# Optimization experiments

Hardware: AMD Instinct MI355X
Metric: run time of the kernel (lower is better)

Reference implementation:

```python
import jax, jax.numpy as jnp
import numpy as np

N, M_CODES, Z_DIM = 4096, 4096, 1024


def setup_inputs() -> dict:
    key = jax.random.key(0)
    k1, k2 = jax.random.split(key)
    z = jax.random.normal(k1, (N, Z_DIM), dtype=jnp.float32)
    e = jax.random.normal(k2, (M_CODES, Z_DIM), dtype=jnp.float32)
    return {"z": z, "e": e}


def reference(z, e):
    # Squared pairwise L2 distances [N, M] via GEMM expansion:
    # ||z_i - e_j||^2 = ||z_i||^2 + ||e_j||^2 - 2 z_i . e_j
    z_sq = jnp.sum(z * z, axis=1)               # [N]
    e_sq = jnp.sum(e * e, axis=1)               # [M]
    cross = jnp.einsum('nd,md->nm', z, e)       # [N, M]
    dist = z_sq[:, None] + e_sq[None, :] - 2.0 * cross  # [N, M]
    # min over dim 0 (over data points N) -> per-code nearest distance [M]
    loss = jnp.mean(jnp.min(dist, axis=0))
    return loss
```

## Files before the change

### kernel.cpp

```cpp
#include <hip/hip_runtime.h>
#include <hip/hip_bf16.h>
#include <stdint.h>

#define N_PTS   4096
#define M_CODES 4096
#define ZDIM    1024
#define BM 128
#define BN 128
#define BK 32

typedef __attribute__((ext_vector_type(8))) short bf16x8;
typedef __attribute__((ext_vector_type(4))) float f32x4;

__device__ __forceinline__ unsigned short f2bf(float f) {
    __hip_bfloat16 h = __float2bfloat16(f);
    return *reinterpret_cast<unsigned short*>(&h);
}

__device__ __forceinline__ unsigned enc_f32(float f) {
    unsigned u = __float_as_uint(f);
    return (u & 0x80000000u) ? ~u : (u | 0x80000000u);
}
__device__ __forceinline__ float dec_f32(unsigned e) {
    unsigned u = (e & 0x80000000u) ? (e ^ 0x80000000u) : ~e;
    return __uint_as_float(u);
}

__global__ __launch_bounds__(256) void prep_kernel(
    const float* __restrict__ z, const float* __restrict__ e,
    unsigned short* __restrict__ zb, unsigned short* __restrict__ eb,
    float* __restrict__ zsq, float* __restrict__ esq,
    unsigned* __restrict__ min_enc) {
    const int row = blockIdx.x;
    const int t = threadIdx.x;
    if (row < 16) min_enc[row * 256 + t] = 0xFFFFFFFFu;

    const float* src;
    unsigned short* dst;
    float* sqp;
    if (row < N_PTS) {
        src = z + (size_t)row * ZDIM; dst = zb + (size_t)row * ZDIM; sqp = zsq + row;
    } else {
        const int r = row - N_PTS;
        src = e + (size_t)r * ZDIM; dst = eb + (size_t)r * ZDIM; sqp = esq + r;
    }
    float4 v = reinterpret_cast<const float4*>(src)[t];
    ushort4 o;
    o.x = f2bf(v.x); o.y = f2bf(v.y); o.z = f2bf(v.z); o.w = f2bf(v.w);
    reinterpret_cast<ushort4*>(dst)[t] = o;
    float s = v.x * v.x + v.y * v.y + v.z * v.z + v.w * v.w;
    #pragma unroll
    for (int off = 32; off > 0; off >>= 1) s += __shfl_down(s, off, 64);
    __shared__ float red[4];
    if ((t & 63) == 0) red[t >> 6] = s;
    __syncthreads();
    if (t == 0) *sqp = red[0] + red[1] + red[2] + red[3];
}

__global__ __launch_bounds__(256) void gemm_min_kernel(
    const unsigned short* __restrict__ zb, const unsigned short* __restrict__ eb,
    const float* __restrict__ zsq, unsigned* __restrict__ min_enc) {
    __shared__ __align__(16) unsigned short As[BM * BK];
    __shared__ __align__(16) unsigned short Bs[BN * BK];
    __shared__ float zsq_s[BM];

    const int t = threadIdx.x;
    const int bx = blockIdx.x;
    const int by = blockIdx.y;
    const int lane = t & 63;
    const int w = t >> 6;
    const int wm = w >> 1, wn = w & 1;
    const int lrow = lane & 15;
    const int q = lane >> 4;

    if (t < BM) zsq_s[t] = zsq[by * BM + t];

    f32x4 acc[4][4];
    #pragma unroll
    for (int i = 0; i < 4; i++)
        #pragma unroll
        for (int j = 0; j < 4; j++) acc[i][j] = (f32x4){0.f, 0.f, 0.f, 0.f};

    const int row0 = (t * 16) >> 6;
    const int kel0 = ((t * 16) & 63) >> 1;
    const int lds_b0 = (t >> 6) * 512;
    const size_t a_base = (size_t)(by * BM) * ZDIM;
    const size_t b_base = (size_t)(bx * BN) * ZDIM;

    for (int k0 = 0; k0 < ZDIM; k0 += BK) {
        const unsigned short* ga0 = zb + a_base + (size_t)row0 * ZDIM + k0 + kel0;
        const unsigned short* gb0 = eb + b_base + (size_t)row0 * ZDIM + k0 + kel0;
        __builtin_amdgcn_global_load_lds(
            (const __attribute__((address_space(1))) void*)ga0,
            (__attribute__((address_space(3))) void*)(As + lds_b0), 16, 0, 0);
        __builtin_amdgcn_global_load_lds(
            (const __attribute__((address_space(1))) void*)(ga0 + (size_t)64 * ZDIM),
            (__attribute__((address_space(3))) void*)(As + 2048 + lds_b0), 16, 0, 0);
        __builtin_amdgcn_global_load_lds(
            (const __attribute__((address_space(1))) void*)gb0,
            (__attribute__((address_space(3))) void*)(Bs + lds_b0), 16, 0, 0);
        __builtin_amdgcn_global_load_lds(
            (const __attribute__((address_space(1))) void*)(gb0 + (size_t)64 * ZDIM),
            (__attribute__((address_space(3))) void*)(Bs + 2048 + lds_b0), 16, 0, 0);
        __syncthreads();

        bf16x8 a[4], b[4];
        #pragma unroll
        for (int am = 0; am < 4; am++)
            a[am] = *(const bf16x8*)(As + (wm * 64 + am * 16 + lrow) * BK + q * 8);
        #pragma unroll
        for (int an = 0; an < 4; an++)
            b[an] = *(const bf16x8*)(Bs + (wn * 64 + an * 16 + lrow) * BK + q * 8);
        #pragma unroll
        for (int am = 0; am < 4; am++)
            #pragma unroll
            for (int an = 0; an < 4; an++)
                acc[am][an] = __builtin_amdgcn_mfma_f32_16x16x32_bf16(
                    a[am], b[an], acc[am][an], 0, 0, 0);
        __syncthreads();
    }

    #pragma unroll
    for (int an = 0; an < 4; an++) {
        float v = 3.4e38f;
        #pragma unroll
        for (int am = 0; am < 4; am++) {
            const int rbase = wm * 64 + am * 16 + q * 4;
            f32x4 c = acc[am][an];
            v = fminf(v, zsq_s[rbase + 0] - 2.f * c[0]);
            v = fminf(v, zsq_s[rbase + 1] - 2.f * c[1]);
            v = fminf(v, zsq_s[rbase + 2] - 2.f * c[2]);
            v = fminf(v, zsq_s[rbase + 3] - 2.f * c[3]);
        }
        v = fminf(v, __shfl_xor(v, 16, 64));
        v = fminf(v, __shfl_xor(v, 32, 64));
        if (q == 0) {
            const int col = bx * BN + wn * 64 + an * 16 + lrow;
            atomicMin(&min_enc[col], enc_f32(v));
        }
    }
}

__global__ __launch_bounds__(256) void finalize_kernel(
    const unsigned* __restrict__ min_enc, const float* __restrict__ esq,
    float* __restrict__ out) {
    const int t = threadIdx.x;
    float s = 0.f;
    #pragma unroll
    for (int i = 0; i < M_CODES / 256; i++) {
        const int j = i * 256 + t;
        s += dec_f32(min_enc[j]) + esq[j];
    }
    #pragma unroll
    for (int off = 32; off > 0; off >>= 1) s += __shfl_down(s, off, 64);
    __shared__ float red[4];
    if ((t & 63) == 0) red[t >> 6] = s;
    __syncthreads();
    if (t == 0) out[0] = (red[0] + red[1] + red[2] + red[3]) * (1.f / M_CODES);
}

extern "C" void kernel_launch(void* const* d_in, const int* in_sizes, int n_in,
                              void* d_out, int out_size, void* d_ws, size_t ws_size,
                              hipStream_t stream) {
    (void)in_sizes; (void)n_in; (void)out_size; (void)ws_size;
    const float* z = (const float*)d_in[0];
    const float* e = (const float*)d_in[1];
    char* ws = (char*)d_ws;
    unsigned short* zb = (unsigned short*)ws;
    unsigned short* eb = (unsigned short*)(ws + ((size_t)8 << 20));
    float* zsq = (float*)(ws + ((size_t)16 << 20));
    float* esq = (float*)(ws + ((size_t)16 << 20) + 4096 * 4);
    unsigned* min_enc = (unsigned*)(ws + ((size_t)16 << 20) + 2 * 4096 * 4);

    prep_kernel<<<dim3(8192), dim3(256), 0, stream>>>(z, e, zb, eb, zsq, esq, min_enc);
    gemm_min_kernel<<<dim3(M_CODES / BN, N_PTS / BM), dim3(256), 0, stream>>>(
        zb, eb, zsq, min_enc);
    finalize_kernel<<<dim3(1), dim3(256), 0, stream>>>(min_enc, esq, (float*)d_out);
}
```

Baseline: 125.0 us.

## Double BK with swizzled LDS, fuse finalize via last-block counter, one-row-per-wave prep

Increases the K tile to 64 so each barrier pair covers twice the MFMA work, and adds an XOR swizzle on LDS chunk placement to avoid bank conflicts on the fragment reads. The per-block column minima are merged in shared memory before a single atomicMin per column. The separate finalize launch is removed, and the last block to finish (tracked by an atomic counter) computes the mean. The prep kernel now processes one row per wave, using a quarter of the blocks and no LDS reduction. This adds threadfence and counter overhead and doubles LDS use per block.

After: 186.0 us. +48.8%, slower.

```diff
diff --git a/kernel.cpp b/kernel.cpp
--- a/kernel.cpp
+++ b/kernel.cpp
@@ -7,7 +7,8 @@
 #define ZDIM    1024
 #define BM 128
 #define BN 128
-#define BK 32
+#define BK 64
+#define NBLOCKS ((N_PTS / BM) * (M_CODES / BN))
 
 typedef __attribute__((ext_vector_type(8))) short bf16x8;
 typedef __attribute__((ext_vector_type(4))) float f32x4;
@@ -30,11 +31,14 @@
     const float* __restrict__ z, const float* __restrict__ e,
     unsigned short* __restrict__ zb, unsigned short* __restrict__ eb,
     float* __restrict__ zsq, float* __restrict__ esq,
-    unsigned* __restrict__ min_enc) {
-    const int row = blockIdx.x;
+    unsigned* __restrict__ min_enc, unsigned* __restrict__ done_counter) {
     const int t = threadIdx.x;
-    if (row < 16) min_enc[row * 256 + t] = 0xFFFFFFFFu;
-
+    const int b = blockIdx.x;
+    if (b < 16) min_enc[b * 256 + t] = 0xFFFFFFFFu;
+    if (b == 16 && t == 0) *done_counter = 0u;
+
+    const int w = t >> 6, lane = t & 63;
+    const int row = b * 4 + w;
     const float* src;
     unsigned short* dst;
     float* sqp;
@@ -44,25 +48,33 @@
         const int r = row - N_PTS;
         src = e + (size_t)r * ZDIM; dst = eb + (size_t)r * ZDIM; sqp = esq + r;
     }
-    float4 v = reinterpret_cast<const float4*>(src)[t];
-    ushort4 o;
-    o.x = f2bf(v.x); o.y = f2bf(v.y); o.z = f2bf(v.z); o.w = f2bf(v.w);
-    reinterpret_cast<ushort4*>(dst)[t] = o;
-    float s = v.x * v.x + v.y * v.y + v.z * v.z + v.w * v.w;
-    #pragma unroll
-    for (int off = 32; off > 0; off >>= 1) s += __shfl_down(s, off, 64);
-    __shared__ float red[4];
-    if ((t & 63) == 0) red[t >> 6] = s;
-    __syncthreads();
-    if (t == 0) *sqp = red[0] + red[1] + red[2] + red[3];
+    const float4* s4 = reinterpret_cast<const float4*>(src);
+    ushort4* d4 = reinterpret_cast<ushort4*>(dst);
+    float s = 0.f;
+    #pragma unroll
+    for (int i = 0; i < 4; i++) {
+        float4 v = s4[i * 64 + lane];
+        ushort4 o;
+        o.x = f2bf(v.x); o.y = f2bf(v.y); o.z = f2bf(v.z); o.w = f2bf(v.w);
+        d4[i * 64 + lane] = o;
+        s += v.x * v.x + v.y * v.y + v.z * v.z + v.w * v.w;
+    }
+    #pragma unroll
+    for (int off = 1; off < 64; off <<= 1) s += __shfl_xor(s, off, 64);
+    if (lane == 0) *sqp = s;
 }
 
 __global__ __launch_bounds__(256) void gemm_min_kernel(
     const unsigned short* __restrict__ zb, const unsigned short* __restrict__ eb,
-    const float* __restrict__ zsq, unsigned* __restrict__ min_enc) {
+    const float* __restrict__ zsq, const float* __restrict__ esq,
+    unsigned* __restrict__ min_enc, unsigned* __restrict__ done_counter,
+    float* __restrict__ out) {
     __shared__ __align__(16) unsigned short As[BM * BK];
     __shared__ __align__(16) unsigned short Bs[BN * BK];
     __shared__ float zsq_s[BM];
+    __shared__ float colmin[2][BN];
+    __shared__ float red[4];
+    __shared__ int last_flag;
 
     const int t = threadIdx.x;
     const int bx = blockIdx.x;
@@ -81,42 +93,49 @@
         #pragma unroll
         for (int j = 0; j < 4; j++) acc[i][j] = (f32x4){0.f, 0.f, 0.f, 0.f};
 
-    const int row0 = (t * 16) >> 6;
-    const int kel0 = ((t * 16) & 63) >> 1;
-    const int lds_b0 = (t >> 6) * 512;
+    const int rloc = t >> 3;
+    const int sw = (t & 7) ^ (rloc & 7);
+    const int ldsw = (t >> 6) * 512;
     const size_t a_base = (size_t)(by * BM) * ZDIM;
     const size_t b_base = (size_t)(bx * BN) * ZDIM;
+    const int swz = lrow & 7;
 
     for (int k0 = 0; k0 < ZDIM; k0 += BK) {
-        const unsigned short* ga0 = zb + a_base + (size_t)row0 * ZDIM + k0 + kel0;
-        const unsigned short* gb0 = eb + b_base + (size_t)row0 * ZDIM + k0 + kel0;
-        __builtin_amdgcn_global_load_lds(
-            (const __attribute__((address_space(1))) void*)ga0,
-            (__attribute__((address_space(3))) void*)(As + lds_b0), 16, 0, 0);
-        __builtin_amdgcn_global_load_lds(
-            (const __attribute__((address_space(1))) void*)(ga0 + (size_t)64 * ZDIM),
-            (__attribute__((address_space(3))) void*)(As + 2048 + lds_b0), 16, 0, 0);
-        __builtin_amdgcn_global_load_lds(
-            (const __attribute__((address_space(1))) void*)gb0,
-            (__attribute__((address_space(3))) void*)(Bs + lds_b0), 16, 0, 0);
-        __builtin_amdgcn_global_load_lds(
-            (const __attribute__((address_space(1))) void*)(gb0 + (size_t)64 * ZDIM),
-            (__attribute__((address_space(3))) void*)(Bs + 2048 + lds_b0), 16, 0, 0);
+        #pragma unroll
+        for (int j = 0; j < 4; j++) {
+            const unsigned short* ga =
+                zb + a_base + (size_t)(j * 32 + rloc) * ZDIM + k0 + sw * 8;
+            const unsigned short* gb =
+                eb + b_base + (size_t)(j * 32 + rloc) * ZDIM + k0 + sw * 8;
+            __builtin_amdgcn_global_load_lds(
+                (const __attribute__((address_space(1))) void*)ga,
+                (__attribute__((address_space(3))) void*)(As + j * 2048 + ldsw), 16, 0, 0);
+            __builtin_amdgcn_global_load_lds(
+                (const __attribute__((address_space(1))) void*)gb,
+                (__attribute__((address_space(3))) void*)(Bs + j * 2048 + ldsw), 16, 0, 0);
+        }
         __syncthreads();
 
-        bf16x8 a[4], b[4];
-        #pragma unroll
-        for (int am = 0; am < 4; am++)
-            a[am] = *(const bf16x8*)(As + (wm * 64 + am * 16 + lrow) * BK + q * 8);
-        #pragma unroll
-        for (int an = 0; an < 4; an++)
-            b[an] = *(const bf16x8*)(Bs + (wn * 64 + an * 16 + lrow) * BK + q * 8);
-        #pragma unroll
-        for (int am = 0; am < 4; am++)
+        #pragma unroll
+        for (int s = 0; s < 2; s++) {
+            bf16x8 a[4], b[4];
             #pragma unroll
-            for (int an = 0; an < 4; an++)
-                acc[am][an] = __builtin_amdgcn_mfma_f32_16x16x32_bf16(
-                    a[am], b[an], acc[am][an], 0, 0, 0);
+            for (int am = 0; am < 4; am++) {
+                const int R = wm * 64 + am * 16 + lrow;
+                a[am] = *(const bf16x8*)(As + R * BK + (((q + 4 * s) ^ swz) * 8));
+            }
+            #pragma unroll
+            for (int an = 0; an < 4; an++) {
+                const int R = wn * 64 + an * 16 + lrow;
+                b[an] = *(const bf16x8*)(Bs + R * BK + (((q + 4 * s) ^ swz) * 8));
+            }
+            #pragma unroll
+            for (int am = 0; am < 4; am++)
+                #pragma unroll
+                for (int an = 0; an < 4; an++)
+                    acc[am][an] = __builtin_amdgcn_mfma_f32_16x16x32_bf16(
+                        a[am], b[an], acc[am][an], 0, 0, 0);
+        }
         __syncthreads();
     }
 
@@ -134,29 +153,37 @@
         }
         v = fminf(v, __shfl_xor(v, 16, 64));
         v = fminf(v, __shfl_xor(v, 32, 64));
-        if (q == 0) {
-            const int col = bx * BN + wn * 64 + an * 16 + lrow;
-            atomicMin(&min_enc[col], enc_f32(v));
-        }
-    }
-}
-
-__global__ __launch_bounds__(256) void finalize_kernel(
-    const unsigned* __restrict__ min_enc, const float* __restrict__ esq,
-    float* __restrict__ out) {
-    const int t = threadIdx.x;
-    float s = 0.f;
-    #pragma unroll
-    for (int i = 0; i < M_CODES / 256; i++) {
-        const int j = i * 256 + t;
-        s += dec_f32(min_enc[j]) + esq[j];
-    }
-    #pragma unroll
-    for (int off = 32; off > 0; off >>= 1) s += __shfl_down(s, off, 64);
-    __shared__ float red[4];
-    if ((t & 63) == 0) red[t >> 6] = s;
+        if (q == 0) colmin[wm][wn * 64 + an * 16 + lrow] = v;
+    }
     __syncthreads();
-    if (t == 0) out[0] = (red[0] + red[1] + red[2] + red[3]) * (1.f / M_CODES);
+    if (t < BN) {
+        const float m = fminf(colmin[0][t], colmin[1][t]);
+        atomicMin(&min_enc[bx * BN + t], enc_f32(m));
+    }
+
+    __threadfence();
+    if (t == 0) {
+        unsigned old = atomicAdd(done_counter, 1u);
+        last_flag = (old == (unsigned)(NBLOCKS - 1));
+    }
+    __syncthreads();
+    if (last_flag) {
+        __threadfence();
+        float s = 0.f;
+        #pragma unroll
+        for (int i = 0; i < M_CODES / 256; i++) {
+            const int j = i * 256 + t;
+            unsigned enc = __hip_atomic_load(&min_enc[j], __ATOMIC_RELAXED,
+                                             __HIP_MEMORY_SCOPE_AGENT);
+            s += dec_f32(enc) + esq[j];
+        }
+        #pragma unroll
+        for (int off = 1; off < 64; off <<= 1) s += __shfl_xor(s, off, 64);
+        if ((t & 63) == 0) red[t >> 6] = s;
+        __syncthreads();
+        if (t == 0)
+            out[0] = (red[0] + red[1] + red[2] + red[3]) * (1.f / M_CODES);
+    }
 }
 
 extern "C" void kernel_launch(void* const* d_in, const int* in_sizes, int n_in,
@@ -171,9 +198,10 @@
     float* zsq = (float*)(ws + ((size_t)16 << 20));
     float* esq = (float*)(ws + ((size_t)16 << 20) + 4096 * 4);
     unsigned* min_enc = (unsigned*)(ws + ((size_t)16 << 20) + 2 * 4096 * 4);
-
-    prep_kernel<<<dim3(8192), dim3(256), 0, stream>>>(z, e, zb, eb, zsq, esq, min_enc);
+    unsigned* done_counter = (unsigned*)(ws + ((size_t)16 << 20) + 3 * 4096 * 4);
+
+    prep_kernel<<<dim3(2048), dim3(256), 0, stream>>>(
+        z, e, zb, eb, zsq, esq, min_enc, done_counter);
     gemm_min_kernel<<<dim3(M_CODES / BN, N_PTS / BM), dim3(256), 0, stream>>>(
-        zb, eb, zsq, min_enc);
-    finalize_kernel<<<dim3(1), dim3(256), 0, stream>>>(min_enc, esq, (float*)d_out);
-}
+        zb, eb, zsq, esq, min_enc, done_counter, (float*)d_out);
+}
```
